# Optimization experiments

Hardware: AMD Instinct MI355X
Metric: run time of the kernel (lower is better)

The kernel has to match this reference:

```python
import jax, jax.numpy as jnp
import numpy as np

B, S, E, H, HD, RD, MP = 2, 2048, 1024, 16, 64, 32, 8  # batch, seq, embed, heads, head_dim, rotary_dim, mp_num


def rotate_every_two(x):
    # x: [..., D] -> interleave (-x_odd, x_even)
    x1 = x[..., ::2]
    x2 = x[..., 1::2]
    return jnp.stack((-x2, x1), axis=-1).reshape(x.shape)


def apply_rotary(x, sin, cos):
    # x: [B,S,H,RD]; sin/cos: [S, RD//2] -> repeat_interleave(2) -> [1,S,1,RD]
    sin = jnp.repeat(sin, 2, axis=-1)[None, :, None, :]
    cos = jnp.repeat(cos, 2, axis=-1)[None, :, None, :]
    return x * cos + rotate_every_two(x) * sin


def setup_inputs() -> dict:
    key = jax.random.key(0)
    k1, k2, k3 = jax.random.split(key, 3)
    return {
        "hidden_states": jax.random.normal(k1, (B, S, E), dtype=jnp.float32),
        "w_qkv": jax.random.normal(k2, (3 * E, E), dtype=jnp.float32) * 0.02,
        "w_out": jax.random.normal(k3, (E, E), dtype=jnp.float32) * 0.02,
    }


def reference(hidden_states, w_qkv, w_out):
    qkv = hidden_states @ w_qkv.T                      # [B,S,3E]
    local = HD * H // MP                               # 128
    qkv = qkv.reshape(B, S, MP, 3 * local)
    # torch.split order in source is (query, value, key)
    q, v, k = jnp.split(qkv, 3, axis=-1)               # each [B,S,MP,local]

    def split_heads(x):
        return x.reshape(B, S, MP, H // MP, HD).reshape(B, S, H, HD)

    q, k, v = split_heads(q), split_heads(k), split_heads(v)  # [B,S,H,HD]

    # fixed sinusoidal rotary embedding over first RD dims
    inv_freq = 1.0 / 10000 ** (jnp.arange(0, RD, 2, dtype=jnp.float32) / RD)
    sinusoid = jnp.arange(S, dtype=jnp.float32)[:, None] * inv_freq[None, :]  # [S, RD//2]
    sin, cos = jnp.sin(sinusoid), jnp.cos(sinusoid)

    q = jnp.concatenate([apply_rotary(q[..., :RD], sin, cos), q[..., RD:]], axis=-1)
    k = jnp.concatenate([apply_rotary(k[..., :RD], sin, cos), k[..., RD:]], axis=-1)

    # [B,H,S,HD]
    q = q.transpose(0, 2, 1, 3)
    k = k.transpose(0, 2, 1, 3)
    v = v.transpose(0, 2, 1, 3)

    scores = jnp.einsum('bhqd,bhkd->bhqk', q, k) / np.float32(np.sqrt(HD))
    causal = jnp.tril(jnp.ones((S, S), dtype=bool))
    scores = jnp.where(causal[None, None], scores, jnp.float32(-1e9))
    attn = jax.nn.softmax(scores.astype(jnp.float32), axis=-1).astype(q.dtype)
    out = jnp.einsum('bhqk,bhkd->bhqd', attn, v)       # [B,H,S,HD]
    out = out.transpose(0, 2, 1, 3).reshape(B, S, E)
    return out @ w_out.T
```

## Files before the change

### kernel.cpp

```cpp
#include <hip/hip_runtime.h>
#include <hip/hip_bf16.h>

typedef __attribute__((ext_vector_type(8))) short short8;
typedef __attribute__((ext_vector_type(4))) float v4f;

#define ASYNC_COPY16(ldsptr, gptr)                                                        \
  __builtin_amdgcn_global_load_lds((const __attribute__((address_space(1))) void*)(gptr), \
                                   (__attribute__((address_space(3))) void*)(ldsptr),     \
                                   16, 0, 0)

__device__ __forceinline__ unsigned short f2bf(float f) {
  unsigned int u = __float_as_uint(f);
  u += 0x7fffu + ((u >> 16) & 1u);
  return (unsigned short)(u >> 16);
}

#define STAGE_SWZ(tt) ((((tt) & 3) ^ (((tt) >> 3) & 3)) * 8)
#define READ_SWZ(kb, lr) (((kb) ^ (((lr) >> 1) & 3)) * 8)

__device__ __forceinline__ void cvt_store(unsigned short* dst, float4 f0, float4 f1) {
  unsigned short v8[8] = {f2bf(f0.x), f2bf(f0.y), f2bf(f0.z), f2bf(f0.w),
                          f2bf(f1.x), f2bf(f1.y), f2bf(f1.z), f2bf(f1.w)};
  *(short8*)dst = *(short8*)v8;
}

__global__ __launch_bounds__(256, 5) void gemm_qkv(const float* __restrict__ A,
                                                   const float* __restrict__ Bm,
                                                   unsigned short* __restrict__ Q,
                                                   unsigned short* __restrict__ Ko,
                                                   unsigned short* __restrict__ Vt) {
  constexpr int Kd = 1024;
  __shared__ __attribute__((aligned(16))) unsigned short As[2 * 128 * 32];
  __shared__ __attribute__((aligned(16))) unsigned short Bs[2 * 64 * 32];
  int t = threadIdx.x;
  int w = t >> 6, lane = t & 63, kb = lane >> 4, lr = lane & 15;
  int m0 = blockIdx.y * 128, n0 = blockIdx.x * 64;
  int wm = (w >> 1) * 64, wn = (w & 1) * 32;
  v4f acc[4][2];
#pragma unroll
  for (int i = 0; i < 4; i++)
#pragma unroll
    for (int j = 0; j < 2; j++) acc[i][j] = (v4f){0.f, 0.f, 0.f, 0.f};
  int ra = m0 + (t >> 2);
  int rb = n0 + (t >> 2);
  int ca = STAGE_SWZ(t);
  int rs = READ_SWZ(kb, lr);
  float4 pa[4], pb[2];
  auto prefetch = [&](int it) {
    int k0 = it * 32;
    const float* a0 = A + (size_t)ra * Kd + k0 + ca;
    const float* a1 = A + (size_t)(ra + 64) * Kd + k0 + ca;
    const float* b0 = Bm + (size_t)rb * Kd + k0 + ca;
    pa[0] = *(const float4*)a0;
    pa[1] = *(const float4*)(a0 + 4);
    pa[2] = *(const float4*)a1;
    pa[3] = *(const float4*)(a1 + 4);
    pb[0] = *(const float4*)b0;
    pb[1] = *(const float4*)(b0 + 4);
  };
  auto commit = [&](int buf) {
    int abase = buf * 4096, bbase = buf * 2048;
    cvt_store(&As[abase + t * 8], pa[0], pa[1]);
    cvt_store(&As[abase + 2048 + t * 8], pa[2], pa[3]);
    cvt_store(&Bs[bbase + t * 8], pb[0], pb[1]);
  };
  prefetch(0);
  commit(0);
  __syncthreads();
  for (int it = 0; it < 32; it++) {
    int acur = (it & 1) * 4096, bcur = (it & 1) * 2048;
    if (it < 31) prefetch(it + 1);
    short8 av[4], bv[2];
#pragma unroll
    for (int i = 0; i < 4; i++)
      av[i] = *(const short8*)&As[acur + (wm + i * 16 + lr) * 32 + rs];
#pragma unroll
    for (int j = 0; j < 2; j++)
      bv[j] = *(const short8*)&Bs[bcur + (wn + j * 16 + lr) * 32 + rs];
#pragma unroll
    for (int i = 0; i < 4; i++)
#pragma unroll
      for (int j = 0; j < 2; j++)
        acc[i][j] = __builtin_amdgcn_mfma_f32_16x16x32_bf16(av[i], bv[j], acc[i][j], 0, 0, 0);
    if (it < 31) commit((it + 1) & 1);
    __syncthreads();
  }
  int X = n0 >> 6;
  int mp = X / 6;
  int sub = X - mp * 6;
  int type = sub >> 1;
  int ii = sub & 1;
  int h = mp * 2 + ii;
  const float qs = 0.125f * 1.4426950408889634f;
  if (type == 1) {
#pragma unroll
    for (int i = 0; i < 4; i++) {
      int row = m0 + wm + i * 16 + kb * 4;
#pragma unroll
      for (int j = 0; j < 2; j++) {
        int dim = wn + j * 16 + lr;
#pragma unroll
        for (int r = 0; r < 4; r++) {
          int m = row + r;
          int b = m >> 11, sl = m & 2047;
          int bh = b * 16 + h;
          int p = (sl & ~31) | ((sl & 15) << 1) | ((sl >> 4) & 1);
          Vt[(size_t)bh * 131072 + (size_t)dim * 2048 + p] = f2bf(acc[i][j][r]);
        }
      }
    }
  } else {
    unsigned short* dst = (type == 0) ? Q : Ko;
    float scale = (type == 0) ? qs : 1.0f;
#pragma unroll
    for (int i = 0; i < 4; i++) {
      int row = m0 + wm + i * 16 + kb * 4;
#pragma unroll
      for (int j = 0; j < 2; j++) {
        int dim = wn + j * 16 + lr;
        float vals[4];
#pragma unroll
        for (int r = 0; r < 4; r++) vals[r] = acc[i][j][r];
        if (dim < 32) {
          int jp = dim >> 1;
          float invf = expf(-(float)jp * 0.57564627324851142f);
#pragma unroll
          for (int r = 0; r < 4; r++) {
            int sl = (row + r) & 2047;
            float ang = (float)sl * invf;
            float sn, cs;
            sincosf(ang, &sn, &cs);
            float partner = __shfl_xor(vals[r], 1);
            float self = vals[r] * cs;
            vals[r] = (lr & 1) ? fmaf(partner, sn, self) : fmaf(-partner, sn, self);
          }
        }
#pragma unroll
        for (int r = 0; r < 4; r++) {
          int m = row + r;
          int b = m >> 11, sl = m & 2047;
          int bh = b * 16 + h;
          dst[(((size_t)(bh * 2048 + sl)) << 6) + dim] = f2bf(vals[r] * scale);
        }
      }
    }
  }
}

__global__ __launch_bounds__(256, 6) void attn_fused(const unsigned short* __restrict__ Qg,
                                                     const unsigned short* __restrict__ Kg,
                                                     const unsigned short* __restrict__ Vtg,
                                                     unsigned short* __restrict__ AO,
                                                     float* __restrict__ PO,
                                                     float* __restrict__ PL) {
  __shared__ __attribute__((aligned(16))) unsigned short Ks[2 * 2048];
  __shared__ __attribute__((aligned(16))) unsigned short Vs[2 * 2048];
  __shared__ __attribute__((aligned(16))) unsigned short Ps[4 * 16 * 40];
  int t = threadIdx.x;
  int w = t >> 6, lane = t & 63, kb = lane >> 4, lr = lane & 15;
  int gid = blockIdx.x;
  int g3 = gid & 7;
  int b2 = (gid >> 3) & 3;
  int z = (gid >> 5) & 7;
  int coset = gid >> 8;
  int bh = g3 * 4 + b2;
  int j = (coset == 0) ? (2 * z)
        : (coset == 1) ? (15 - 2 * z)
        : (coset == 2) ? (16 + z)
        : (coset == 3) ? (31 - z)
        : (coset == 4) ? (32 + z)
                       : (47 - z);
  int qtile, kt0, kt1, mode;
  if (j < 16)      { qtile = j;      mode = 0; kt0 = 0;          kt1 = 2 * qtile + 2; }
  else if (j < 32) { qtile = j;      mode = 1; kt0 = 0;          kt1 = qtile + 1; }
  else             { qtile = j - 16; mode = 2; kt0 = qtile + 1;  kt1 = 2 * qtile + 2; }
  int m0 = qtile * 64;
  const unsigned short* Qb = Qg + (size_t)bh * 2048 * 64;
  const unsigned short* Kb = Kg + (size_t)bh * 2048 * 64;
  const unsigned short* Vb = Vtg + (size_t)bh * 64 * 2048;

  short8 aq0 = *(const short8*)(Qb + (size_t)(m0 + w * 16 + lr) * 64 + kb * 8);
  short8 aq1 = *(const short8*)(Qb + (size_t)(m0 + w * 16 + lr) * 64 + 32 + kb * 8);

  v4f acc[4];
  float lp[4];
#pragma unroll
  for (int n = 0; n < 4; n++) acc[n] = (v4f){0.f, 0.f, 0.f, 0.f};
#pragma unroll
  for (int r = 0; r < 4; r++) lp[r] = 0.f;

  int mrow = w * 16 + kb * 4;

  int kc = t >> 5, krow_s = t & 31;
  int vc = t >> 6, vd = t & 63;
  auto stage = [&](int kt, int buf) {
    int base = buf * 2048;
    ASYNC_COPY16(&Ks[base + t * 8], Kb + (size_t)(kt * 32 + krow_s) * 64 + kc * 8);
    ASYNC_COPY16(&Vs[base + t * 8], Vb + (size_t)vd * 2048 + kt * 32 + vc * 8);
  };

  stage(kt0, 0);
  __syncthreads();

  unsigned short* Pw = &Ps[w * 640];
  int niter = kt1 - kt0;
  for (int it = 0; it < niter; it++) {
    int kt = kt0 + it;
    int cur = (it & 1) * 2048;
    if (it + 1 < niter) stage(kt + 1, (it + 1) & 1);
    v4f sc[2];
#pragma unroll
    for (int n2 = 0; n2 < 2; n2++) {
      int krow = n2 * 16 + lr;
      short8 bk0 = *(const short8*)&Ks[cur + (kb * 32 + krow) * 8];
      short8 bk1 = *(const short8*)&Ks[cur + ((kb + 4) * 32 + krow) * 8];
      v4f zz = (v4f){0.f, 0.f, 0.f, 0.f};
      zz = __builtin_amdgcn_mfma_f32_16x16x32_bf16(aq0, bk0, zz, 0, 0, 0);
      zz = __builtin_amdgcn_mfma_f32_16x16x32_bf16(aq1, bk1, zz, 0, 0, 0);
      sc[n2] = zz;
    }
    if (kt >= 2 * qtile) {
#pragma unroll
      for (int n2 = 0; n2 < 2; n2++)
#pragma unroll
        for (int r = 0; r < 4; r++) {
          int key = kt * 32 + n2 * 16 + lr;
          if (key > m0 + mrow + r) sc[n2][r] = -1e30f;
        }
    }
#pragma unroll
    for (int r = 0; r < 4; r++) {
      float p0 = exp2f(sc[0][r]);
      float p1 = exp2f(sc[1][r]);
      lp[r] += p0 + p1;
      __hip_bfloat162 pb = __float22bfloat162_rn(float2{p0, p1});
      *(__hip_bfloat162*)&Pw[(mrow & 15) * 40 + r * 40 + lr * 2] = pb;
    }
    short8 ap = *(const short8*)&Pw[lr * 40 + kb * 8];
#pragma unroll
    for (int dt = 0; dt < 4; dt++) {
      int d = dt * 16 + lr;
      short8 bv = *(const short8*)&Vs[cur + (kb * 64 + d) * 8];
      acc[dt] = __builtin_amdgcn_mfma_f32_16x16x32_bf16(ap, bv, acc[dt], 0, 0, 0);
    }
    __syncthreads();
  }
  float s[4];
#pragma unroll
  for (int r = 0; r < 4; r++) {
    s[r] = lp[r];
#pragma unroll
    for (int off = 1; off < 16; off <<= 1) s[r] += __shfl_xor(s[r], off);
  }
  if (mode == 0) {
    int b = bh >> 4, h = bh & 15;
#pragma unroll
    for (int r = 0; r < 4; r++) {
      float inv = 1.0f / s[r];
      int qrow = m0 + mrow + r;
#pragma unroll
      for (int dt = 0; dt < 4; dt++)
        AO[(size_t)(b * 2048 + qrow) * 1024 + h * 64 + dt * 16 + lr] = f2bf(acc[dt][r] * inv);
    }
  } else {
    int hf = mode - 1;
    size_t pbase = ((size_t)hf * 512 + bh * 16 + (qtile - 16)) * 4096;
    size_t plbase = (size_t)hf * 32768 + (bh * 16 + (qtile - 16)) * 64;
#pragma unroll
    for (int r = 0; r < 4; r++) {
      if (lr == 0) PL[plbase + mrow + r] = s[r];
#pragma unroll
      for (int dt = 0; dt < 4; dt++)
        PO[pbase + (size_t)(mrow + r) * 64 + dt * 16 + lr] = acc[dt][r];
    }
  }
}

__global__ __launch_bounds__(256, 4) void gemm_out(const unsigned short* __restrict__ AO,
                                                   const float* __restrict__ PO,
                                                   const float* __restrict__ PL,
                                                   const float* __restrict__ Bm,
                                                   float* __restrict__ C) {
  constexpr int Kd = 1024, Nd = 1024;
  __shared__ __attribute__((aligned(16))) unsigned short As[2 * 64 * 32];
  __shared__ __attribute__((aligned(16))) unsigned short Bs[2 * 64 * 32];
  int t = threadIdx.x;
  int w = t >> 6, lane = t & 63, kb = lane >> 4, lr = lane & 15;
  int m0 = blockIdx.y * 64, n0 = blockIdx.x * 64;
  bool comb = (blockIdx.y >> 4) & 1;
  int wm = (w >> 1) * 32, wn = (w & 1) * 32;
  v4f acc[2][2];
#pragma unroll
  for (int i = 0; i < 2; i++)
#pragma unroll
    for (int j = 0; j < 2; j++) acc[i][j] = (v4f){0.f, 0.f, 0.f, 0.f};
  int ra = m0 + (t >> 2);
  int rb = n0 + (t >> 2);
  int ca = STAGE_SWZ(t);
  int rs = READ_SWZ(kb, lr);
  int b = ra >> 11, qrow = ra & 2047;
  int q16 = (qrow >> 6) - 16, lrow = qrow & 63;
  float4 pb[2], pa0[2], pa1[2];
  float lsum = 1.0f;
  auto prefetch = [&](int it, int buf) {
    int k0 = it * 32;
    const float* b0 = Bm + (size_t)rb * Kd + k0 + ca;
    pb[0] = *(const float4*)b0;
    pb[1] = *(const float4*)(b0 + 4);
    if (comb) {
      int h = k0 >> 6, d0 = (k0 & 32) + ca;
      size_t idx = ((size_t)((b * 16 + h) * 16 + q16) * 64 + lrow) * 64 + d0;
      pa0[0] = *(const float4*)&PO[idx];
      pa0[1] = *(const float4*)&PO[idx + 4];
      pa1[0] = *(const float4*)&PO[2097152 + idx];
      pa1[1] = *(const float4*)&PO[2097152 + idx + 4];
      int pli = ((b * 16 + h) * 16 + q16) * 64 + lrow;
      lsum = PL[pli] + PL[32768 + pli];
    } else {
      ASYNC_COPY16(&As[buf * 2048 + t * 8], AO + (size_t)ra * Kd + k0 + ca);
    }
  };
  auto commit = [&](int buf) {
    cvt_store(&Bs[buf * 2048 + t * 8], pb[0], pb[1]);
    if (comb) {
      float inv = 1.0f / lsum;
      float4 f0, f1;
      f0.x = (pa0[0].x + pa1[0].x) * inv; f0.y = (pa0[0].y + pa1[0].y) * inv;
      f0.z = (pa0[0].z + pa1[0].z) * inv; f0.w = (pa0[0].w + pa1[0].w) * inv;
      f1.x = (pa0[1].x + pa1[1].x) * inv; f1.y = (pa0[1].y + pa1[1].y) * inv;
      f1.z = (pa0[1].z + pa1[1].z) * inv; f1.w = (pa0[1].w + pa1[1].w) * inv;
      cvt_store(&As[buf * 2048 + t * 8], f0, f1);
    }
  };
  prefetch(0, 0);
  commit(0);
  __syncthreads();
  for (int it = 0; it < 32; it++) {
    int cur = (it & 1) * 2048;
    if (it < 31) prefetch(it + 1, (it + 1) & 1);
    short8 av[2], bv[2];
#pragma unroll
    for (int i = 0; i < 2; i++) av[i] = *(const short8*)&As[cur + (wm + i * 16 + lr) * 32 + rs];
#pragma unroll
    for (int j = 0; j < 2; j++) bv[j] = *(const short8*)&Bs[cur + (wn + j * 16 + lr) * 32 + rs];
#pragma unroll
    for (int i = 0; i < 2; i++)
#pragma unroll
      for (int j = 0; j < 2; j++)
        acc[i][j] = __builtin_amdgcn_mfma_f32_16x16x32_bf16(av[i], bv[j], acc[i][j], 0, 0, 0);
    if (it < 31) commit((it + 1) & 1);
    __syncthreads();
  }
#pragma unroll
  for (int i = 0; i < 2; i++) {
    int row = m0 + wm + i * 16 + kb * 4;
#pragma unroll
    for (int j = 0; j < 2; j++) {
      int col = n0 + wn + j * 16 + lr;
#pragma unroll
      for (int r = 0; r < 4; r++) C[(size_t)(row + r) * Nd + col] = acc[i][j][r];
    }
  }
}

extern "C" void kernel_launch(void* const* d_in, const int* in_sizes, int n_in,
                              void* d_out, int out_size, void* d_ws, size_t ws_size,
                              hipStream_t stream) {
  const float* hidden = (const float*)d_in[0];
  const float* w_qkv = (const float*)d_in[1];
  const float* w_out = (const float*)d_in[2];
  float* out = (float*)d_out;
  char* ws = (char*)d_ws;
  unsigned short* Qb = (unsigned short*)(ws + (16ull << 20));
  unsigned short* Kb = (unsigned short*)(ws + (24ull << 20));
  unsigned short* Vt = (unsigned short*)(ws + (32ull << 20));
  unsigned short* AO = (unsigned short*)(ws + (40ull << 20));
  float* PO = (float*)(ws + (48ull << 20));
  float* PL = (float*)(ws + (64ull << 20));

  gemm_qkv<<<dim3(48, 32), 256, 0, stream>>>(hidden, w_qkv, Qb, Kb, Vt);
  attn_fused<<<1536, 256, 0, stream>>>(Qb, Kb, Vt, AO, PO, PL);
  gemm_out<<<dim3(16, 64), 256, 0, stream>>>(AO, PO, PL, w_out, out);
}
```

Baseline: 222.0 us.

## Pre-convert QKV GEMM inputs to bf16 and stage tiles via async LDS loads

```diff
diff --git a/kernel.cpp b/kernel.cpp
--- a/kernel.cpp
+++ b/kernel.cpp
@@ -15,6 +15,20 @@
   return (unsigned short)(u >> 16);
 }
 
+__global__ void convert_in(const float* __restrict__ h, const float* __restrict__ wq,
+                           unsigned short* __restrict__ ho, unsigned short* __restrict__ wqo) {
+  int i = (blockIdx.x * blockDim.x + threadIdx.x) * 4;
+  const float* src;
+  unsigned short* dst;
+  int j;
+  if (i < 4194304) { src = h; dst = ho; j = i; }
+  else { src = wq; dst = wqo; j = i - 4194304; }
+  float4 v = *(const float4*)(src + j);
+  ushort4 o;
+  o.x = f2bf(v.x); o.y = f2bf(v.y); o.z = f2bf(v.z); o.w = f2bf(v.w);
+  *(ushort4*)(dst + j) = o;
+}
+
 #define STAGE_SWZ(tt) ((((tt) & 3) ^ (((tt) >> 3) & 3)) * 8)
 #define READ_SWZ(kb, lr) (((kb) ^ (((lr) >> 1) & 3)) * 8)
 
@@ -24,14 +38,14 @@
   *(short8*)dst = *(short8*)v8;
 }
 
-__global__ __launch_bounds__(256, 5) void gemm_qkv(const float* __restrict__ A,
-                                                   const float* __restrict__ Bm,
+__global__ __launch_bounds__(256, 6) void gemm_qkv(const unsigned short* __restrict__ A,
+                                                   const unsigned short* __restrict__ Bm,
                                                    unsigned short* __restrict__ Q,
                                                    unsigned short* __restrict__ Ko,
                                                    unsigned short* __restrict__ Vt) {
   constexpr int Kd = 1024;
-  __shared__ __attribute__((aligned(16))) unsigned short As[2 * 128 * 32];
-  __shared__ __attribute__((aligned(16))) unsigned short Bs[2 * 64 * 32];
+  __shared__ __attribute__((aligned(16))) unsigned short As[128 * 32];
+  __shared__ __attribute__((aligned(16))) unsigned short Bs[64 * 32];
   int t = threadIdx.x;
   int w = t >> 6, lane = t & 63, kb = lane >> 4, lr = lane & 15;
   int m0 = blockIdx.y * 128, n0 = blockIdx.x * 64;
@@ -45,44 +59,21 @@
   int rb = n0 + (t >> 2);
   int ca = STAGE_SWZ(t);
   int rs = READ_SWZ(kb, lr);
-  float4 pa[4], pb[2];
-  auto prefetch = [&](int it) {
-    int k0 = it * 32;
-    const float* a0 = A + (size_t)ra * Kd + k0 + ca;
-    const float* a1 = A + (size_t)(ra + 64) * Kd + k0 + ca;
-    const float* b0 = Bm + (size_t)rb * Kd + k0 + ca;
-    pa[0] = *(const float4*)a0;
-    pa[1] = *(const float4*)(a0 + 4);
-    pa[2] = *(const float4*)a1;
-    pa[3] = *(const float4*)(a1 + 4);
-    pb[0] = *(const float4*)b0;
-    pb[1] = *(const float4*)(b0 + 4);
-  };
-  auto commit = [&](int buf) {
-    int abase = buf * 4096, bbase = buf * 2048;
-    cvt_store(&As[abase + t * 8], pa[0], pa[1]);
-    cvt_store(&As[abase + 2048 + t * 8], pa[2], pa[3]);
-    cvt_store(&Bs[bbase + t * 8], pb[0], pb[1]);
-  };
-  prefetch(0);
-  commit(0);
-  __syncthreads();
-  for (int it = 0; it < 32; it++) {
-    int acur = (it & 1) * 4096, bcur = (it & 1) * 2048;
-    if (it < 31) prefetch(it + 1);
+  for (int k0 = 0; k0 < Kd; k0 += 32) {
+    ASYNC_COPY16(&As[t * 8],        A + (size_t)ra * Kd + k0 + ca);
+    ASYNC_COPY16(&As[2048 + t * 8], A + (size_t)(ra + 64) * Kd + k0 + ca);
+    ASYNC_COPY16(&Bs[t * 8],        Bm + (size_t)rb * Kd + k0 + ca);
+    __syncthreads();
     short8 av[4], bv[2];
 #pragma unroll
-    for (int i = 0; i < 4; i++)
-      av[i] = *(const short8*)&As[acur + (wm + i * 16 + lr) * 32 + rs];
-#pragma unroll
-    for (int j = 0; j < 2; j++)
-      bv[j] = *(const short8*)&Bs[bcur + (wn + j * 16 + lr) * 32 + rs];
+    for (int i = 0; i < 4; i++) av[i] = *(const short8*)&As[(wm + i * 16 + lr) * 32 + rs];
+#pragma unroll
+    for (int j = 0; j < 2; j++) bv[j] = *(const short8*)&Bs[(wn + j * 16 + lr) * 32 + rs];
 #pragma unroll
     for (int i = 0; i < 4; i++)
 #pragma unroll
       for (int j = 0; j < 2; j++)
         acc[i][j] = __builtin_amdgcn_mfma_f32_16x16x32_bf16(av[i], bv[j], acc[i][j], 0, 0, 0);
-    if (it < 31) commit((it + 1) & 1);
     __syncthreads();
   }
   int X = n0 >> 6;
@@ -371,6 +362,8 @@
   const float* w_out = (const float*)d_in[2];
   float* out = (float*)d_out;
   char* ws = (char*)d_ws;
+  unsigned short* hid_bf = (unsigned short*)(ws);
+  unsigned short* wqkv_bf = (unsigned short*)(ws + (8ull << 20));
   unsigned short* Qb = (unsigned short*)(ws + (16ull << 20));
   unsigned short* Kb = (unsigned short*)(ws + (24ull << 20));
   unsigned short* Vt = (unsigned short*)(ws + (32ull << 20));
@@ -378,7 +371,8 @@
   float* PO = (float*)(ws + (48ull << 20));
   float* PL = (float*)(ws + (64ull << 20));
 
-  gemm_qkv<<<dim3(48, 32), 256, 0, stream>>>(hidden, w_qkv, Qb, Kb, Vt);
+  convert_in<<<7168, 256, 0, stream>>>(hidden, w_qkv, hid_bf, wqkv_bf);
+  gemm_qkv<<<dim3(48, 32), 256, 0, stream>>>(hid_bf, wqkv_bf, Qb, Kb, Vt);
   attn_fused<<<1536, 256, 0, stream>>>(Qb, Kb, Vt, AO, PO, PL);
   gemm_out<<<dim3(16, 64), 256, 0, stream>>>(AO, PO, PL, w_out, out);
 }
```

Result: faster. 207.7 us (-6.4%).
